# Performance work log

Hardware: AMD Instinct MI355X
Metric: run time of the kernel (lower is better)

## Reference

```python
import jax, jax.numpy as jnp
import numpy as np

DIM = 2048
NUM_HEADS = 16
NUM_KV_HEADS = 4
HEAD_DIM = DIM // NUM_HEADS  # 128
ROPE_BASE = 10000.0
CLIP = 31.0
BLOCK = 128


def fake_quant(w):
    """Blockwise int-ish fake quantization, steady QAT state (ratio=1, clip=31, no noise)."""
    out_f, in_f = w.shape
    pad = (-in_f) % BLOCK
    wp = jnp.pad(w, ((0, 0), (0, pad)))
    wb = wp.reshape(-1, BLOCK)
    # scale computed under no_grad in torch -> stop_gradient
    bmax = jnp.max(jnp.abs(wb), axis=1)
    s = jnp.maximum(bmax / CLIP, 1e-12).astype(jnp.float16)
    s = jnp.maximum(s, jnp.finfo(jnp.float16).tiny).astype(jnp.float32)
    s = jax.lax.stop_gradient(s)[:, None]
    ws = wb / s
    q = ws - jax.lax.stop_gradient(ws) + jax.lax.stop_gradient(
        jnp.round(jnp.clip(ws, -(CLIP + 1.0), CLIP)))  # STE
    qw = (q * s).reshape(out_f, in_f + pad)
    return qw[:, :in_f] if pad > 0 else qw


def rms_norm(x):
    eps = jnp.finfo(x.dtype).eps
    return x * jax.lax.rsqrt(jnp.mean(x * x, axis=-1, keepdims=True) + eps)


def rope_tables(seqlen, dtype):
    inv_freq = 1.0 / (ROPE_BASE ** (jnp.arange(0, HEAD_DIM, 2, dtype=jnp.float32) / HEAD_DIM))
    freqs = jnp.outer(jnp.arange(seqlen, dtype=jnp.float32), inv_freq)  # [S, hd/2]
    return jnp.cos(freqs).astype(dtype), jnp.sin(freqs).astype(dtype)


def apply_rotary(x, cos, sin):
    # x: [B,H,S,hd]; cos/sin: [S,hd/2]
    half = x.shape[-1] // 2
    x1, x2 = x[..., :half], x[..., half:]
    return jnp.concatenate((x1 * cos + x2 * sin, -x1 * sin + x2 * cos), axis=-1)


def setup_inputs() -> dict:
    key = jax.random.key(0)
    ks = jax.random.split(key, 6)
    kv_dim = NUM_KV_HEADS * HEAD_DIM
    std = DIM ** -0.5
    return {
        "x": jax.random.normal(ks[0], (2, 2048, DIM), dtype=jnp.float32),
        "Wq": jax.random.normal(ks[1], (DIM, DIM), dtype=jnp.float32) * std,
        "Wk": jax.random.normal(ks[2], (kv_dim, DIM), dtype=jnp.float32) * std,
        "Wv": jax.random.normal(ks[3], (kv_dim, DIM), dtype=jnp.float32) * std,
        "Wproj": jax.random.normal(ks[4], (DIM, DIM), dtype=jnp.float32) * std,
        "q_gain": jnp.full((NUM_HEADS,), 1.0, dtype=jnp.float32),
    }


def reference(x, Wq, Wk, Wv, Wproj, q_gain):
    B, S, D = x.shape
    H, KV, hd = NUM_HEADS, NUM_KV_HEADS, HEAD_DIM
    q = (x @ fake_quant(Wq).T).reshape(B, S, H, hd).transpose(0, 2, 1, 3)   # [B,H,S,hd]
    k = (x @ fake_quant(Wk).T).reshape(B, S, KV, hd).transpose(0, 2, 1, 3)  # [B,KV,S,hd]
    v = (x @ fake_quant(Wv).T).reshape(B, S, KV, hd).transpose(0, 2, 1, 3)
    q = rms_norm(q)
    k = rms_norm(k)
    cos, sin = rope_tables(S, q.dtype)
    q = apply_rotary(q, cos, sin)
    k = apply_rotary(k, cos, sin)
    q = q * q_gain[None, :, None, None]
    # GQA: expand kv heads
    rep = H // KV
    k = jnp.repeat(k, rep, axis=1)  # [B,H,S,hd]
    v = jnp.repeat(v, rep, axis=1)
    scale = 1.0 / jnp.sqrt(jnp.asarray(hd, dtype=q.dtype))
    scores = jnp.einsum("bhqd,bhkd->bhqk", q, k) * scale
    causal = jnp.tril(jnp.ones((S, S), dtype=bool))
    scores = jnp.where(causal, scores, jnp.asarray(-jnp.inf, dtype=scores.dtype))
    attn = jax.nn.softmax(scores, axis=-1)
    y = jnp.einsum("bhqk,bhkd->bhqd", attn, v)  # [B,H,S,hd]
    y = y.transpose(0, 2, 1, 3).reshape(B, S, D)
    return y @ fake_quant(Wproj).T
```

## Files before the change

### kernel.cpp

```cpp
#include <hip/hip_runtime.h>
#include <hip/hip_bf16.h>
#include <hip/hip_fp16.h>

#define SEQ    2048
#define DMODEL 2048
#define NH     16
#define NKV    4
#define HD     128
#define NTOT   3072
#define MROWS  4096

typedef __attribute__((ext_vector_type(4))) float f32x4;
typedef __attribute__((ext_vector_type(8))) __bf16 bf16x8;
typedef __attribute__((ext_vector_type(8))) unsigned short u16x8;
typedef __attribute__((ext_vector_type(4))) unsigned short u16x4;

__device__ __forceinline__ void async_copy16(const void* g, void* l) {
  __builtin_amdgcn_global_load_lds(
      (const __attribute__((address_space(1))) void*)g,
      (__attribute__((address_space(3))) void*)l, 16, 0, 0);
}

__device__ __forceinline__ unsigned short fto16(float f) {
  __hip_bfloat16 h = __float2bfloat16(f);
  return *(unsigned short*)&h;
}

__device__ __forceinline__ float b2f(unsigned short u) {
  unsigned int t = (unsigned int)u << 16;
  float f;
  __builtin_memcpy(&f, &t, 4);
  return f;
}

__global__ __launch_bounds__(256) void fq_kernel(const float* __restrict__ Wq,
                                                 const float* __restrict__ Wk,
                                                 const float* __restrict__ Wv,
                                                 const float* __restrict__ Wp,
                                                 unsigned short* __restrict__ Wcat,
                                                 unsigned short* __restrict__ Wpq) {
  int g = blockIdx.x * 4 + (threadIdx.x >> 6);
  int lane = threadIdx.x & 63;
  const float* W;
  unsigned short* out;
  int blk;
  if (g < 32768)      { W = Wq; out = Wcat;                          blk = g; }
  else if (g < 40960) { W = Wk; out = Wcat + (size_t)2048 * 2048;    blk = g - 32768; }
  else if (g < 49152) { W = Wv; out = Wcat + (size_t)2560 * 2048;    blk = g - 40960; }
  else                { W = Wp; out = Wpq;                           blk = g - 49152; }
  const float* p = W + (size_t)blk * 128 + lane * 2;
  float w0 = p[0], w1 = p[1];
  float m = fmaxf(fabsf(w0), fabsf(w1));
#pragma unroll
  for (int o = 32; o; o >>= 1) m = fmaxf(m, __shfl_xor(m, o));
  float s = fmaxf(m / 31.0f, 1e-12f);
  s = __half2float(__float2half(s));
  s = fmaxf(s, 6.103515625e-05f);
  float q0 = rintf(fminf(fmaxf(w0 / s, -32.0f), 31.0f)) * s;
  float q1 = rintf(fminf(fmaxf(w1 / s, -32.0f), 31.0f)) * s;
  unsigned short* o16 = out + (size_t)blk * 128 + lane * 2;
  o16[0] = fto16(q0);
  o16[1] = fto16(q1);
}

__global__ __launch_bounds__(256) void conv_kernel(const float* __restrict__ in,
                                                   unsigned short* __restrict__ out,
                                                   int n) {
  int i = (blockIdx.x * blockDim.x + threadIdx.x) * 4;
  if (i >= n) return;
  float4 v = *(const float4*)(in + i);
  ushort4 o;
  o.x = fto16(v.x); o.y = fto16(v.y); o.z = fto16(v.z); o.w = fto16(v.w);
  *(ushort4*)(out + i) = o;
}

#define BM 128
#define BN 128
#define BK 32
template <typename OT>
__global__ __launch_bounds__(256) void gemm_bt(const unsigned short* __restrict__ A,
                                               const unsigned short* __restrict__ Bm,
                                               OT* __restrict__ C,
                                               int M, int N, int K) {
  __shared__ unsigned short As[BM * BK];
  __shared__ unsigned short Bs[BN * BK];
  const int tid = threadIdx.x;
  const int wave = tid >> 6, lane = tid & 63;
  const int quad = lane >> 4, l16 = lane & 15;
  const int m0 = blockIdx.x * BM, n0 = blockIdx.y * BN;
  const int wm = (wave >> 1) * 64, wn = (wave & 1) * 64;
  const int sr = lane >> 2, sc = (lane & 3) * 8;

  const unsigned short* Ag = A + (size_t)m0 * K;
  const unsigned short* Bg = Bm + (size_t)n0 * K;

  f32x4 acc[4][4];
#pragma unroll
  for (int i = 0; i < 4; i++)
#pragma unroll
    for (int j = 0; j < 4; j++) acc[i][j] = f32x4{0.f, 0.f, 0.f, 0.f};

  const int seg0 = wave * 2, seg1 = wave * 2 + 1;
  unsigned short* lA0 = &As[seg0 * 16 * BK];
  unsigned short* lA1 = &As[seg1 * 16 * BK];
  unsigned short* lB0 = &Bs[seg0 * 16 * BK];
  unsigned short* lB1 = &Bs[seg1 * 16 * BK];
  const unsigned short* gA0 = Ag + (size_t)(seg0 * 16 + sr) * K + sc;
  const unsigned short* gA1 = Ag + (size_t)(seg1 * 16 + sr) * K + sc;
  const unsigned short* gB0 = Bg + (size_t)(seg0 * 16 + sr) * K + sc;
  const unsigned short* gB1 = Bg + (size_t)(seg1 * 16 + sr) * K + sc;

  for (int k0 = 0; k0 < K; k0 += BK) {
    __syncthreads();
    async_copy16(gA0 + k0, lA0);
    async_copy16(gA1 + k0, lA1);
    async_copy16(gB0 + k0, lB0);
    async_copy16(gB1 + k0, lB1);
    __syncthreads();
    bf16x8 af[4], bf[4];
#pragma unroll
    for (int t = 0; t < 4; t++)
      af[t] = *(const bf16x8*)&As[(wm + t * 16 + l16) * BK + quad * 8];
#pragma unroll
    for (int t = 0; t < 4; t++)
      bf[t] = *(const bf16x8*)&Bs[(wn + t * 16 + l16) * BK + quad * 8];
#pragma unroll
    for (int i = 0; i < 4; i++)
#pragma unroll
      for (int j = 0; j < 4; j++)
        acc[i][j] = __builtin_amdgcn_mfma_f32_16x16x32_bf16(af[i], bf[j], acc[i][j], 0, 0, 0);
  }
#pragma unroll
  for (int i = 0; i < 4; i++) {
    int row_base = m0 + wm + i * 16 + quad * 4;
#pragma unroll
    for (int j = 0; j < 4; j++) {
      int col = n0 + wn + j * 16 + l16;
#pragma unroll
      for (int r = 0; r < 4; r++) {
        if constexpr (sizeof(OT) == 2)
          C[(size_t)(row_base + r) * N + col] = fto16(acc[i][j][r]);
        else
          C[(size_t)(row_base + r) * N + col] = acc[i][j][r];
      }
    }
  }
}

#define QSCALE 0.12751791437524245f
__global__ __launch_bounds__(256) void normrope_kernel(const unsigned short* __restrict__ qkvb,
                                                       const float* __restrict__ qgain,
                                                       unsigned short* __restrict__ qbuf,
                                                       unsigned short* __restrict__ kbuf) {
  const int i = blockIdx.x;
  const int bz = i >> 11, tok = i & 2047;
  const int wave = threadIdx.x >> 6, lane = threadIdx.x & 63;
  const unsigned short* row = qkvb + (size_t)i * NTOT;

  double invf = pow(10000.0, -(double)(2 * lane) / 128.0);
  float freq = (float)((double)tok * invf);
  float cs = cosf(freq), sn = sinf(freq);

  for (int slot = wave; slot < 20; slot += 4) {
    if (slot < 16) {
      int hh = slot;
      const unsigned short* src = row + hh * HD;
      float x1 = b2f(src[lane]), x2 = b2f(src[lane + 64]);
      float ss = x1 * x1 + x2 * x2;
#pragma unroll
      for (int o = 32; o; o >>= 1) ss += __shfl_xor(ss, o);
      float rn = rsqrtf(ss * (1.0f / 128.0f) + 1.1920929e-07f);
      float n1 = x1 * rn, n2 = x2 * rn;
      float g = qgain[hh] * QSCALE;
      unsigned short* dst = qbuf + ((size_t)(bz * NH + hh) * SEQ + tok) * HD;
      dst[lane]      = fto16((n1 * cs + n2 * sn) * g);
      dst[lane + 64] = fto16((-n1 * sn + n2 * cs) * g);
    } else {
      int hh = slot - 16;
      const unsigned short* src = row + DMODEL + hh * HD;
      float x1 = b2f(src[lane]), x2 = b2f(src[lane + 64]);
      float ss = x1 * x1 + x2 * x2;
#pragma unroll
      for (int o = 32; o; o >>= 1) ss += __shfl_xor(ss, o);
      float rn = rsqrtf(ss * (1.0f / 128.0f) + 1.1920929e-07f);
      float n1 = x1 * rn, n2 = x2 * rn;
      unsigned short* dst = kbuf + ((size_t)(bz * NKV + hh) * SEQ + tok) * HD;
      dst[lane]      = fto16(n1 * cs + n2 * sn);
      dst[lane + 64] = fto16(-n1 * sn + n2 * cs);
    }
  }
}

__global__ __launch_bounds__(256) void vtrans_kernel(const unsigned short* __restrict__ qkvb,
                                                     unsigned short* __restrict__ vtb) {
  __shared__ unsigned short T[64 * 72];
  const int s0 = blockIdx.x * 64;
  const int d0 = blockIdx.y * 64;
  const int bz = blockIdx.z >> 2, h = blockIdx.z & 3;
  const int tid = threadIdx.x;
#pragma unroll
  for (int i = 0; i < 2; ++i) {
    int c = i * 256 + tid;
    int s = c >> 3, ch = c & 7;
    const unsigned short* src =
        qkvb + (size_t)(bz * SEQ + s0 + s) * NTOT + DMODEL + 512 + h * HD + d0 + ch * 8;
    *(u16x8*)&T[s * 72 + ch * 8] = *(const u16x8*)src;
  }
  __syncthreads();
  unsigned short* outg = vtb + (size_t)(bz * NKV + h) * HD * SEQ;
#pragma unroll
  for (int i = 0; i < 2; ++i) {
    int c = i * 256 + tid;
    int d = c >> 3, sc = c & 7;
    u16x8 v;
#pragma unroll
    for (int j = 0; j < 8; ++j) v[j] = T[(sc * 8 + j) * 72 + d];
    *(u16x8*)(outg + (size_t)(d0 + d) * SEQ + s0 + sc * 8) = v;
  }
}

__global__ __launch_bounds__(512, 4) void attn_kernel(const unsigned short* __restrict__ qb,
                                                      const unsigned short* __restrict__ kb,
                                                      const unsigned short* __restrict__ vtb,
                                                      unsigned short* __restrict__ yb) {
  __shared__ unsigned short Ks[64 * 128];
  __shared__ unsigned short Vt[128 * 64];
  __shared__ unsigned short Ps[8][16 * 64];

  const int bx = blockIdx.x;
  const int h = blockIdx.y;
  const int bz = blockIdx.z;
  const int qt = bz ? bx : (15 - bx);
  const int tid = threadIdx.x;
  const int wave = tid >> 6, lane = tid & 63;
  const int quad = lane >> 4, l16 = lane & 15;
  const int q0 = qt * 128;
  const int base = q0 + wave * 16;
  const int kdiag = base >> 6;

  const unsigned short* qg = qb + (size_t)(bz * NH + h) * SEQ * HD;
  const unsigned short* kg = kb + (size_t)(bz * NKV + (h >> 2)) * SEQ * HD;
  const unsigned short* vg = vtb + (size_t)(bz * NKV + (h >> 2)) * HD * SEQ;
  unsigned short* psw = &Ps[wave][0];

  bf16x8 qf[4];
#pragma unroll
  for (int ds = 0; ds < 4; ++ds)
    qf[ds] = *(const bf16x8*)(qg + (size_t)(base + l16) * HD + ds * 32 + quad * 8);

  f32x4 oacc[8];
#pragma unroll
  for (int j = 0; j < 8; ++j) oacc[j] = f32x4{0.f, 0.f, 0.f, 0.f};
  float m_i = -__builtin_inff();
  float l_i = 0.f;

  const int krw = tid >> 4, kgr = tid & 15;
  const int vdw = tid >> 3, vgr = tid & 7;

  const int nkt = 2 * qt + 2;

  u16x8 pk[2], pv[2];
#pragma unroll
  for (int i = 0; i < 2; ++i)
    pk[i] = *(const u16x8*)(kg + (size_t)(i * 32 + krw) * HD + kgr * 8);
#pragma unroll
  for (int i = 0; i < 2; ++i)
    pv[i] = *(const u16x8*)(vg + (size_t)(i * 64 + vdw) * SEQ + vgr * 8);

  for (int kt = 0; kt < nkt; ++kt) {
#pragma unroll
    for (int i = 0; i < 2; ++i) {
      int row = i * 32 + krw;
      *(u16x8*)&Ks[row * 128 + ((kgr ^ (row & 15)) << 3)] = pk[i];
    }
#pragma unroll
    for (int i = 0; i < 2; ++i) {
      int d = i * 64 + vdw;
      *(u16x8*)&Vt[d * 64 + ((vgr ^ (d & 7)) << 3)] = pv[i];
    }
    __syncthreads();

    if (kt + 1 < nkt) {
#pragma unroll
      for (int i = 0; i < 2; ++i)
        pk[i] = *(const u16x8*)(kg + (size_t)((kt + 1) * 64 + i * 32 + krw) * HD + kgr * 8);
#pragma unroll
      for (int i = 0; i < 2; ++i)
        pv[i] = *(const u16x8*)(vg + (size_t)(i * 64 + vdw) * SEQ + (kt + 1) * 64 + vgr * 8);
    }

    if (kt <= kdiag) {
      f32x4 st[4];
#pragma unroll
      for (int mt = 0; mt < 4; ++mt) st[mt] = f32x4{0.f, 0.f, 0.f, 0.f};
#pragma unroll
      for (int mt = 0; mt < 4; ++mt)
#pragma unroll
        for (int ds = 0; ds < 4; ++ds) {
          bf16x8 kf = *(const bf16x8*)&Ks[(mt * 16 + l16) * 128 + ((((ds << 2) + quad) ^ l16) << 3)];
          st[mt] = __builtin_amdgcn_mfma_f32_16x16x32_bf16(kf, qf[ds], st[mt], 0, 0, 0);
        }

      const int qrow = base + l16;
      float p[4][4];
      float mx = -__builtin_inff();
      if (kt == kdiag) {
#pragma unroll
        for (int mt = 0; mt < 4; ++mt)
#pragma unroll
          for (int r = 0; r < 4; ++r) {
            int kp = kt * 64 + mt * 16 + quad * 4 + r;
            float v = (kp <= qrow) ? st[mt][r] : -__builtin_inff();
            p[mt][r] = v;
            mx = fmaxf(mx, v);
          }
      } else {
#pragma unroll
        for (int mt = 0; mt < 4; ++mt)
#pragma unroll
          for (int r = 0; r < 4; ++r) {
            p[mt][r] = st[mt][r];
            mx = fmaxf(mx, st[mt][r]);
          }
      }
      mx = fmaxf(mx, __shfl_xor(mx, 16));
      mx = fmaxf(mx, __shfl_xor(mx, 32));
      float mnew = fmaxf(m_i, mx);
      float rs = 0.f;
#pragma unroll
      for (int mt = 0; mt < 4; ++mt)
#pragma unroll
        for (int r = 0; r < 4; ++r) {
          float e = exp2f(p[mt][r] - mnew);
          p[mt][r] = e;
          rs += e;
        }
      rs += __shfl_xor(rs, 16);
      rs += __shfl_xor(rs, 32);
      if (__any(mnew > m_i)) {
        float a = exp2f(m_i - mnew);
#pragma unroll
        for (int j = 0; j < 8; ++j) oacc[j] *= a;
        l_i = l_i * a + rs;
      } else {
        l_i += rs;
      }
      m_i = mnew;

#pragma unroll
      for (int mt = 0; mt < 4; ++mt) {
        u16x4 w;
#pragma unroll
        for (int r = 0; r < 4; ++r) w[r] = fto16(p[mt][r]);
        int g = mt * 2 + (quad >> 1);
        *(u16x4*)&psw[l16 * 64 + ((g ^ (l16 & 7)) << 3) + (quad & 1) * 4] = w;
      }

      __asm__ volatile("s_waitcnt lgkmcnt(0)" ::: "memory");

#pragma unroll
      for (int c = 0; c < 2; ++c) {
        bf16x8 pf = *(const bf16x8*)&psw[l16 * 64 + ((((c << 2) + quad) ^ (l16 & 7)) << 3)];
#pragma unroll
        for (int mt = 0; mt < 8; ++mt) {
          bf16x8 vf = *(const bf16x8*)&Vt[(mt * 16 + l16) * 64 + ((((c << 2) + quad) ^ (l16 & 7)) << 3)];
          oacc[mt] = __builtin_amdgcn_mfma_f32_16x16x32_bf16(vf, pf, oacc[mt], 0, 0, 0);
        }
      }
    }
    __syncthreads();
  }

  {
    float il = 1.0f / l_i;
    int qrow = base + l16;
#pragma unroll
    for (int mt = 0; mt < 8; ++mt) {
      u16x4 o;
#pragma unroll
      for (int r = 0; r < 4; ++r) o[r] = fto16(oacc[mt][r] * il);
      *(u16x4*)&yb[(size_t)(bz * SEQ + qrow) * DMODEL + h * HD + mt * 16 + quad * 4] = o;
    }
  }
}

extern "C" void kernel_launch(void* const* d_in, const int* in_sizes, int n_in,
                              void* d_out, int out_size, void* d_ws, size_t ws_size,
                              hipStream_t stream) {
  (void)in_sizes; (void)n_in; (void)out_size; (void)ws_size;
  const float* x  = (const float*)d_in[0];
  const float* Wq = (const float*)d_in[1];
  const float* Wk = (const float*)d_in[2];
  const float* Wv = (const float*)d_in[3];
  const float* Wp = (const float*)d_in[4];
  const float* qg = (const float*)d_in[5];
  float* out = (float*)d_out;
  char* ws = (char*)d_ws;

  unsigned short* xb   = (unsigned short*)(ws + 0);
  unsigned short* Wcat = (unsigned short*)(ws + 16777216);
  unsigned short* Wpq  = (unsigned short*)(ws + 29360128);
  unsigned short* qkvb = (unsigned short*)(ws + 37748736);
  unsigned short* qbuf = (unsigned short*)(ws + 62914560);
  unsigned short* kbuf = (unsigned short*)(ws + 79691776);
  unsigned short* vtb  = (unsigned short*)(ws + 83886080);
  unsigned short* yb   = xb;

  fq_kernel<<<81920 / 4, 256, 0, stream>>>(Wq, Wk, Wv, Wp, Wcat, Wpq);
  conv_kernel<<<8388608 / 1024, 256, 0, stream>>>(x, xb, 8388608);
  gemm_bt<unsigned short><<<dim3(32, 24), 256, 0, stream>>>(xb, Wcat, qkvb, MROWS, NTOT, DMODEL);
  normrope_kernel<<<MROWS, 256, 0, stream>>>(qkvb, qg, qbuf, kbuf);
  vtrans_kernel<<<dim3(32, 2, 8), 256, 0, stream>>>(qkvb, vtb);
  attn_kernel<<<dim3(16, NH, 2), 512, 0, stream>>>(qbuf, kbuf, vtb, yb);
  gemm_bt<float><<<dim3(32, 16), 256, 0, stream>>>(yb, Wpq, out, MROWS, DMODEL, DMODEL);
}
```

Before: 331.3 us.

## Double-buffer attention K tiles via async LDS copies and widen GEMM K-tile

```diff
diff --git a/kernel.cpp b/kernel.cpp
--- a/kernel.cpp
+++ b/kernel.cpp
@@ -76,20 +76,25 @@
 
 #define BM 128
 #define BN 128
-#define BK 32
+#define BK 64
 template <typename OT>
-__global__ __launch_bounds__(256) void gemm_bt(const unsigned short* __restrict__ A,
-                                               const unsigned short* __restrict__ Bm,
-                                               OT* __restrict__ C,
-                                               int M, int N, int K) {
+__global__ __launch_bounds__(256, 3) void gemm_bt(const unsigned short* __restrict__ A,
+                                                  const unsigned short* __restrict__ Bm,
+                                                  OT* __restrict__ C,
+                                                  int M, int N, int K) {
   __shared__ unsigned short As[BM * BK];
   __shared__ unsigned short Bs[BN * BK];
   const int tid = threadIdx.x;
   const int wave = tid >> 6, lane = tid & 63;
   const int quad = lane >> 4, l16 = lane & 15;
-  const int m0 = blockIdx.x * BM, n0 = blockIdx.y * BN;
+
+  int wg = blockIdx.y * gridDim.x + blockIdx.x;
+  int nwg = gridDim.x * gridDim.y;
+  int cpx = nwg >> 3;
+  int swz = (wg & 7) * cpx + (wg >> 3);
+  int bxs = swz % gridDim.x, bys = swz / gridDim.x;
+  const int m0 = bxs * BM, n0 = bys * BN;
   const int wm = (wave >> 1) * 64, wn = (wave & 1) * 64;
-  const int sr = lane >> 2, sc = (lane & 3) * 8;
 
   const unsigned short* Ag = A + (size_t)m0 * K;
   const unsigned short* Bg = Bm + (size_t)n0 * K;
@@ -100,35 +105,35 @@
 #pragma unroll
     for (int j = 0; j < 4; j++) acc[i][j] = f32x4{0.f, 0.f, 0.f, 0.f};
 
-  const int seg0 = wave * 2, seg1 = wave * 2 + 1;
-  unsigned short* lA0 = &As[seg0 * 16 * BK];
-  unsigned short* lA1 = &As[seg1 * 16 * BK];
-  unsigned short* lB0 = &Bs[seg0 * 16 * BK];
-  unsigned short* lB1 = &Bs[seg1 * 16 * BK];
-  const unsigned short* gA0 = Ag + (size_t)(seg0 * 16 + sr) * K + sc;
-  const unsigned short* gA1 = Ag + (size_t)(seg1 * 16 + sr) * K + sc;
-  const unsigned short* gB0 = Bg + (size_t)(seg0 * 16 + sr) * K + sc;
-  const unsigned short* gB1 = Bg + (size_t)(seg1 * 16 + sr) * K + sc;
+  const int srow = tid >> 3;
+  const int sg8 = (((lane & 7) ^ (lane >> 3))) * 8;
+  const unsigned short* gA = Ag + (size_t)srow * K + sg8;
+  const unsigned short* gB = Bg + (size_t)srow * K + sg8;
+  unsigned short* lA = &As[wave * 512];
+  unsigned short* lB = &Bs[wave * 512];
 
   for (int k0 = 0; k0 < K; k0 += BK) {
     __syncthreads();
-    async_copy16(gA0 + k0, lA0);
-    async_copy16(gA1 + k0, lA1);
-    async_copy16(gB0 + k0, lB0);
-    async_copy16(gB1 + k0, lB1);
+#pragma unroll
+    for (int c = 0; c < 4; ++c) async_copy16(gA + (size_t)c * 32 * K + k0, lA + c * 2048);
+#pragma unroll
+    for (int c = 0; c < 4; ++c) async_copy16(gB + (size_t)c * 32 * K + k0, lB + c * 2048);
     __syncthreads();
-    bf16x8 af[4], bf[4];
-#pragma unroll
-    for (int t = 0; t < 4; t++)
-      af[t] = *(const bf16x8*)&As[(wm + t * 16 + l16) * BK + quad * 8];
-#pragma unroll
-    for (int t = 0; t < 4; t++)
-      bf[t] = *(const bf16x8*)&Bs[(wn + t * 16 + l16) * BK + quad * 8];
-#pragma unroll
-    for (int i = 0; i < 4; i++)
-#pragma unroll
-      for (int j = 0; j < 4; j++)
-        acc[i][j] = __builtin_amdgcn_mfma_f32_16x16x32_bf16(af[i], bf[j], acc[i][j], 0, 0, 0);
+#pragma unroll
+    for (int kk = 0; kk < 2; ++kk) {
+      bf16x8 af[4], bf[4];
+#pragma unroll
+      for (int t = 0; t < 4; t++)
+        af[t] = *(const bf16x8*)&As[(wm + t * 16 + l16) * BK + ((((kk << 2) + quad) ^ (l16 & 7)) << 3)];
+#pragma unroll
+      for (int t = 0; t < 4; t++)
+        bf[t] = *(const bf16x8*)&Bs[(wn + t * 16 + l16) * BK + ((((kk << 2) + quad) ^ (l16 & 7)) << 3)];
+#pragma unroll
+      for (int i = 0; i < 4; i++)
+#pragma unroll
+        for (int j = 0; j < 4; j++)
+          acc[i][j] = __builtin_amdgcn_mfma_f32_16x16x32_bf16(af[i], bf[j], acc[i][j], 0, 0, 0);
+    }
   }
 #pragma unroll
   for (int i = 0; i < 4; i++) {
@@ -223,7 +228,7 @@
                                                       const unsigned short* __restrict__ kb,
                                                       const unsigned short* __restrict__ vtb,
                                                       unsigned short* __restrict__ yb) {
-  __shared__ unsigned short Ks[64 * 128];
+  __shared__ unsigned short Ks[2][64 * 128];
   __shared__ unsigned short Vt[128 * 64];
   __shared__ unsigned short Ps[8][16 * 64];
 
@@ -254,52 +259,57 @@
   float m_i = -__builtin_inff();
   float l_i = 0.f;
 
-  const int krw = tid >> 4, kgr = tid & 15;
+  const int krow0 = wave * 4 + (lane >> 4);
+  const int ksrcg = (lane & 15) ^ (krow0 & 15);
+  const unsigned short* kgK = kg + (size_t)krow0 * HD + ksrcg * 8;
+
   const int vdw = tid >> 3, vgr = tid & 7;
 
   const int nkt = 2 * qt + 2;
 
-  u16x8 pk[2], pv[2];
-#pragma unroll
-  for (int i = 0; i < 2; ++i)
-    pk[i] = *(const u16x8*)(kg + (size_t)(i * 32 + krw) * HD + kgr * 8);
+  async_copy16(kgK, &Ks[0][wave * 512]);
+  async_copy16(kgK + (size_t)32 * HD, &Ks[0][4096 + wave * 512]);
+  u16x8 pv[2];
 #pragma unroll
   for (int i = 0; i < 2; ++i)
     pv[i] = *(const u16x8*)(vg + (size_t)(i * 64 + vdw) * SEQ + vgr * 8);
 
   for (int kt = 0; kt < nkt; ++kt) {
-#pragma unroll
-    for (int i = 0; i < 2; ++i) {
-      int row = i * 32 + krw;
-      *(u16x8*)&Ks[row * 128 + ((kgr ^ (row & 15)) << 3)] = pk[i];
-    }
+    __syncthreads();
 #pragma unroll
     for (int i = 0; i < 2; ++i) {
       int d = i * 64 + vdw;
       *(u16x8*)&Vt[d * 64 + ((vgr ^ (d & 7)) << 3)] = pv[i];
     }
-    __syncthreads();
-
     if (kt + 1 < nkt) {
-#pragma unroll
-      for (int i = 0; i < 2; ++i)
-        pk[i] = *(const u16x8*)(kg + (size_t)((kt + 1) * 64 + i * 32 + krw) * HD + kgr * 8);
+      const unsigned short* s = kgK + (size_t)(kt + 1) * 64 * HD;
+      async_copy16(s, &Ks[(kt + 1) & 1][wave * 512]);
+      async_copy16(s + (size_t)32 * HD, &Ks[(kt + 1) & 1][4096 + wave * 512]);
+    }
+    __asm__ volatile("s_waitcnt lgkmcnt(0)" ::: "memory");
+    __builtin_amdgcn_sched_barrier(0);
+    __asm__ volatile("s_barrier" ::: "memory");
+
+    if (kt + 1 < nkt) {
 #pragma unroll
       for (int i = 0; i < 2; ++i)
         pv[i] = *(const u16x8*)(vg + (size_t)(i * 64 + vdw) * SEQ + (kt + 1) * 64 + vgr * 8);
     }
 
     if (kt <= kdiag) {
+      const unsigned short* Kc = Ks[kt & 1];
       f32x4 st[4];
 #pragma unroll
       for (int mt = 0; mt < 4; ++mt) st[mt] = f32x4{0.f, 0.f, 0.f, 0.f};
+      __builtin_amdgcn_s_setprio(1);
 #pragma unroll
       for (int mt = 0; mt < 4; ++mt)
 #pragma unroll
         for (int ds = 0; ds < 4; ++ds) {
-          bf16x8 kf = *(const bf16x8*)&Ks[(mt * 16 + l16) * 128 + ((((ds << 2) + quad) ^ l16) << 3)];
+          bf16x8 kf = *(const bf16x8*)&Kc[(mt * 16 + l16) * 128 + ((((ds << 2) + quad) ^ l16) << 3)];
           st[mt] = __builtin_amdgcn_mfma_f32_16x16x32_bf16(kf, qf[ds], st[mt], 0, 0, 0);
         }
+      __builtin_amdgcn_s_setprio(0);
 
       const int qrow = base + l16;
       float p[4][4];
@@ -325,7 +335,7 @@
       }
       mx = fmaxf(mx, __shfl_xor(mx, 16));
       mx = fmaxf(mx, __shfl_xor(mx, 32));
-      float mnew = fmaxf(m_i, mx);
+      float mnew = (mx > m_i + 8.f) ? mx : m_i;
       float rs = 0.f;
 #pragma unroll
       for (int mt = 0; mt < 4; ++mt)
@@ -337,15 +347,15 @@
         }
       rs += __shfl_xor(rs, 16);
       rs += __shfl_xor(rs, 32);
-      if (__any(mnew > m_i)) {
+      if (mnew != m_i) {
         float a = exp2f(m_i - mnew);
 #pragma unroll
         for (int j = 0; j < 8; ++j) oacc[j] *= a;
         l_i = l_i * a + rs;
+        m_i = mnew;
       } else {
         l_i += rs;
       }
-      m_i = mnew;
 
 #pragma unroll
       for (int mt = 0; mt < 4; ++mt) {
@@ -358,6 +368,7 @@
 
       __asm__ volatile("s_waitcnt lgkmcnt(0)" ::: "memory");
 
+      __builtin_amdgcn_s_setprio(1);
 #pragma unroll
       for (int c = 0; c < 2; ++c) {
         bf16x8 pf = *(const bf16x8*)&psw[l16 * 64 + ((((c << 2) + quad) ^ (l16 & 7)) << 3)];
@@ -367,8 +378,8 @@
           oacc[mt] = __builtin_amdgcn_mfma_f32_16x16x32_bf16(vf, pf, oacc[mt], 0, 0, 0);
         }
       }
-    }
-    __syncthreads();
+      __builtin_amdgcn_s_setprio(0);
+    }
   }
 
   {
```

New measurement: 309.4 us. -6.6%, faster.
